# Performance work log

Hardware: AMD Instinct MI355X
Metric: run time of the kernel (lower is better)

Reference implementation:

```python
import jax, jax.numpy as jnp
import numpy as np

HEADS = 8
HEAD_DIM = 64
EPS = 1e-5


def setup_inputs() -> dict:
    key = jax.random.key(0)
    k1, k2, k3 = jax.random.split(key, 3)
    dim, hidden = 512, HEADS * HEAD_DIM
    x = jax.random.normal(k1, (8, dim, 64, 64), dtype=jnp.float32)
    w_qkv = jax.random.normal(k2, (hidden * 3, dim), dtype=jnp.float32) * (dim ** -0.5)
    w_out = jax.random.normal(k3, (dim, hidden), dtype=jnp.float32) * (hidden ** -0.5)
    b_out = jnp.zeros((dim,), dtype=jnp.float32)
    g = jnp.ones((dim,), dtype=jnp.float32)
    return {"x": x, "w_qkv": w_qkv, "w_out": w_out, "b_out": b_out, "g": g}


def reference(x, w_qkv, w_out, b_out, g):
    b, c, h, w = x.shape
    n = h * w
    scale = HEAD_DIM ** -0.5
    xf = x.reshape(b, c, n)  # 1x1 conv == channel matmul
    qkv = jnp.einsum('oc,bcn->bon', w_qkv, xf)
    q, k, v = jnp.split(qkv, 3, axis=1)
    def to_heads(t):
        return t.reshape(b, HEADS, HEAD_DIM, n)
    q, k, v = to_heads(q), to_heads(k), to_heads(v)
    q = jax.nn.softmax(q, axis=-2) * scale   # softmax over head_dim
    k = jax.nn.softmax(k, axis=-1)           # softmax over tokens
    v = v / n
    # context: (B,H,d,d) = k (B,H,d,N) @ v^T (B,H,N,e)
    context = jnp.einsum('bhdn,bhen->bhde', k, v)
    # out: context^T (e,d) @ q (d,N) -> (B,H,e,N)
    out = jnp.einsum('bhde,bhdn->bhen', context, q)
    out = out.reshape(b, HEADS * HEAD_DIM, n)
    y = jnp.einsum('co,bon->bcn', w_out, out) + b_out[None, :, None]
    # channel LayerNorm (mean/var over dim=1, biased var, scale g only)
    mean = jnp.mean(y, axis=1, keepdims=True)
    var = jnp.var(y, axis=1, keepdims=True)
    y = (y - mean) * jax.lax.rsqrt(var + EPS) * g[None, :, None]
    return y.reshape(b, c, h, w)
```

## Files before the change

### kernel.cpp

```cpp
#include <hip/hip_runtime.h>
#include <math.h>

#define BB 8
#define NN 4096
#define CD 512
#define HH 8
#define DD 64
#define OC3 1536
#define NSPLIT 16

typedef _Float16 f16;
typedef _Float16 half8 __attribute__((ext_vector_type(8)));
typedef _Float16 half4v __attribute__((ext_vector_type(4)));
typedef float f32x4 __attribute__((ext_vector_type(4)));

__device__ __forceinline__ void gload_lds16(const void* g, void* l) {
    __builtin_amdgcn_global_load_lds(
        (const __attribute__((address_space(1))) unsigned int*)g,
        (__attribute__((address_space(3))) unsigned int*)l, 16, 0, 0);
}

__global__ __launch_bounds__(256) void split_w_kernel(
    const float* __restrict__ w, f16* __restrict__ wh, f16* __restrict__ wl)
{
    int idx = blockIdx.x * 256 + threadIdx.x;
    float4 v = ((const float4*)w)[idx];
    float a[4] = {v.x, v.y, v.z, v.w};
    half4v h, l;
    #pragma unroll
    for (int i = 0; i < 4; ++i) {
        float s = a[i] * 64.f;
        f16 hh = (f16)s;
        h[i] = hh;
        l[i] = (f16)(s - (float)hh);
    }
    *(half4v*)(&wh[(long)idx * 4]) = h;
    *(half4v*)(&wl[(long)idx * 4]) = l;
}

__global__ __launch_bounds__(256) void split_x_kernel(
    const float* __restrict__ x, f16* __restrict__ xth, f16* __restrict__ xtl)
{
    __shared__ float tile[64][65];
    int b = blockIdx.z;
    int n0 = blockIdx.x * 64, c0 = blockIdx.y * 64;
    const float* xb = x + ((long)b * CD + c0) * NN + n0;
    int t = threadIdx.x;
    int tr = t >> 6, tc = t & 63;
    #pragma unroll
    for (int i = 0; i < 16; ++i)
        tile[tr + i * 4][tc] = xb[(long)(tr + i * 4) * NN + tc];
    __syncthreads();

    int nl = t >> 3, ck = (t & 7) * 8;
    long obase = ((long)b * NN + n0) * CD + c0;
    #pragma unroll
    for (int p = 0; p < 2; ++p) {
        int n = nl + p * 32;
        half8 h, l;
        #pragma unroll
        for (int j = 0; j < 8; ++j) {
            float s = tile[ck + j][n] * 16.f;
            f16 hv = (f16)s;
            h[j] = hv;
            l[j] = (f16)(s - (float)hv);
        }
        *(half8*)(&xth[obase + (long)n * CD + ck]) = h;
        *(half8*)(&xtl[obase + (long)n * CD + ck]) = l;
    }
}

#define STAGE(Lb, k0s)  do {                                                   \
    long kb_ = (long)(k0s) * 2;                                                \
    _Pragma("unroll")                                                          \
    for (int c_ = 0; c_ < 2; ++c_) {                                           \
        long rowoff_ = (long)(rb0 + c_ * 16) * 1024;                           \
        long ldsoff_ = (long)(rb0 + c_ * 16) * 64;                             \
        gload_lds16(gA_h + rowoff_ + kb_ + g_lane, (Lb) + 0 * 8192 + ldsoff_); \
        gload_lds16(gA_l + rowoff_ + kb_ + g_lane, (Lb) + 1 * 8192 + ldsoff_); \
        gload_lds16(gB_h + rowoff_ + kb_ + g_lane, (Lb) + 2 * 8192 + ldsoff_); \
        gload_lds16(gB_l + rowoff_ + kb_ + g_lane, (Lb) + 3 * 8192 + ldsoff_); \
    } } while (0)

__global__ __launch_bounds__(256) void mfma_gemm_kernel(
    const f16* __restrict__ Ah, const f16* __restrict__ Al, long sA,
    const f16* __restrict__ Bh, const f16* __restrict__ Bl, long sB,
    float* __restrict__ Cp, long sC, int ldC,
    const float* __restrict__ bias, const float* __restrict__ inv_sc,
    float base_sc, int fuseqv)
{
    __shared__ f16 lds[2][4][128 * 32];
    int bz = blockIdx.z;
    int n0 = blockIdx.x * 128, m0 = blockIdx.y * 128;
    int t = threadIdx.x;
    int lane = t & 63, wid = t >> 6;
    int wy = wid >> 1, wx = wid & 1;

    int cl = (lane & 3) ^ ((lane >> 3) & 3);
    long g_lane = (long)(lane >> 2) * 1024 + (long)cl * 16;

    const char* gA_h = (const char*)(Ah + bz * sA) + (long)m0 * 1024;
    const char* gA_l = (const char*)(Al + bz * sA) + (long)m0 * 1024;
    const char* gB_h = (const char*)(Bh + bz * sB) + (long)n0 * 1024;
    const char* gB_l = (const char*)(Bl + bz * sB) + (long)n0 * 1024;

    char* L0 = (char*)&lds[0][0][0];
    int rb0 = wid * 32;

    int cp = (lane >> 4) ^ (((lane & 15) >> 1) & 3);
    long offA = (long)(wy * 64 + (lane & 15)) * 64 + (long)cp * 16;
    long offB = (long)(wx * 64 + (lane & 15)) * 64 + (long)cp * 16;

    f32x4 acc[4][4];
    #pragma unroll
    for (int i = 0; i < 4; ++i)
        #pragma unroll
        for (int j = 0; j < 4; ++j)
            acc[i][j] = (f32x4){0.f, 0.f, 0.f, 0.f};

    STAGE(L0, 0);
    asm volatile("s_waitcnt vmcnt(0)" ::: "memory");
    __syncthreads();

    for (int s = 0; s < 16; ++s) {
        char* Lc = L0 + ((s & 1) << 15);
        if (s < 15) {
            char* Ln = L0 + (((s + 1) & 1) << 15);
            STAGE(Ln, (s + 1) * 32);
        }

        half8 ah[4], al[4], bh[4], bl[4];
        #pragma unroll
        for (int i = 0; i < 4; ++i) {
            ah[i] = *(const half8*)(Lc + 0 * 8192 + offA + i * 1024);
            al[i] = *(const half8*)(Lc + 1 * 8192 + offA + i * 1024);
            bh[i] = *(const half8*)(Lc + 2 * 8192 + offB + i * 1024);
            bl[i] = *(const half8*)(Lc + 3 * 8192 + offB + i * 1024);
        }
        #pragma unroll
        for (int i = 0; i < 4; ++i)
            #pragma unroll
            for (int j = 0; j < 4; ++j) {
                acc[i][j] = __builtin_amdgcn_mfma_f32_16x16x32_f16(ah[i], bh[j], acc[i][j], 0, 0, 0);
                acc[i][j] = __builtin_amdgcn_mfma_f32_16x16x32_f16(ah[i], bl[j], acc[i][j], 0, 0, 0);
                acc[i][j] = __builtin_amdgcn_mfma_f32_16x16x32_f16(al[i], bh[j], acc[i][j], 0, 0, 0);
            }

        asm volatile("s_waitcnt vmcnt(0)" ::: "memory");
        __syncthreads();
    }

    int colb = n0 + wx * 64 + (lane & 15);
    int rowb = m0 + wy * 64 + ((lane >> 4) << 2);

    if (fuseqv && m0 < 512) {
        int h = (m0 >> 6) + wy;
        f16* qh_b = (f16*)(Cp + (long)bz * sC);
        f16* ql_b = qh_b + (long)CD * NN;
        #pragma unroll
        for (int i = 0; i < 4; ++i)
            #pragma unroll
            for (int j = 0; j < 4; ++j)
                #pragma unroll
                for (int r = 0; r < 4; ++r)
                    acc[i][j][r] *= base_sc;
        #pragma unroll
        for (int j = 0; j < 4; ++j) {
            float mx = -INFINITY;
            #pragma unroll
            for (int i = 0; i < 4; ++i)
                #pragma unroll
                for (int r = 0; r < 4; ++r)
                    mx = fmaxf(mx, acc[i][j][r]);
            mx = fmaxf(mx, __shfl_xor(mx, 16));
            mx = fmaxf(mx, __shfl_xor(mx, 32));
            float sum = 0.f;
            #pragma unroll
            for (int i = 0; i < 4; ++i)
                #pragma unroll
                for (int r = 0; r < 4; ++r) {
                    float e = expf(acc[i][j][r] - mx);
                    acc[i][j][r] = e;
                    sum += e;
                }
            sum += __shfl_xor(sum, 16);
            sum += __shfl_xor(sum, 32);
            float rj = 32.f / sum;
            long nj = colb + j * 16;
            long off = nj * CD + h * 64 + ((lane >> 4) << 2);
            #pragma unroll
            for (int i = 0; i < 4; ++i) {
                half4v hh, ll;
                #pragma unroll
                for (int r = 0; r < 4; ++r) {
                    float v = acc[i][j][r] * rj;
                    f16 hv = (f16)v;
                    hh[r] = hv;
                    ll[r] = (f16)(v - (float)hv);
                }
                *(half4v*)(qh_b + off + i * 16) = hh;
                *(half4v*)(ql_b + off + i * 16) = ll;
            }
        }
        return;
    }

    if (fuseqv && m0 >= 1024) {
        f16* vhp = (f16*)(Cp + (long)bz * sC + 2L * CD * NN);
        f16* vlp = vhp + (long)CD * NN;
        float vsc = base_sc * 16.f;
        #pragma unroll
        for (int i = 0; i < 4; ++i)
            #pragma unroll
            for (int j = 0; j < 4; ++j)
                #pragma unroll
                for (int r = 0; r < 4; ++r) {
                    long row = rowb + i * 16 + r - 1024;
                    float val = acc[i][j][r] * vsc;
                    f16 hv = (f16)val;
                    vhp[row * NN + colb + j * 16] = hv;
                    vlp[row * NN + colb + j * 16] = (f16)(val - (float)hv);
                }
        return;
    }

    float* outp = Cp + bz * sC;
    float mult = base_sc * (inv_sc ? inv_sc[bz] : 1.f);
    #pragma unroll
    for (int i = 0; i < 4; ++i)
        #pragma unroll
        for (int j = 0; j < 4; ++j)
            #pragma unroll
            for (int r = 0; r < 4; ++r) {
                int row = rowb + i * 16 + r;
                float bb = bias ? bias[row] : 0.f;
                outp[(long)row * ldC + colb + j * 16] = acc[i][j][r] * mult + bb;
            }
}

__global__ __launch_bounds__(256) void softmax_k_kernel(
    const float* __restrict__ qkv, f16* __restrict__ ksp)
{
    int row = blockIdx.x;
    int b = row >> 9;
    int hd = row & (CD - 1);
    const float* base = qkv + ((long)b * OC3 + CD + hd) * NN;
    f16* khb = ksp + (long)b * 2 * CD * NN + (long)hd * NN;
    f16* klb = khb + (long)CD * NN;
    int t = threadIdx.x;

    float v[16];
    #pragma unroll
    for (int i = 0; i < 16; ++i) v[i] = base[t + i * 256];

    __shared__ float red[256];
    float mx = -INFINITY;
    #pragma unroll
    for (int i = 0; i < 16; ++i) mx = fmaxf(mx, v[i]);
    red[t] = mx; __syncthreads();
    for (int off = 128; off > 0; off >>= 1) {
        if (t < off) red[t] = fmaxf(red[t], red[t + off]);
        __syncthreads();
    }
    mx = red[0]; __syncthreads();

    float s = 0.f;
    #pragma unroll
    for (int i = 0; i < 16; ++i) {
        v[i] = expf(v[i] - mx);
        s += v[i];
    }
    red[t] = s; __syncthreads();
    for (int off = 128; off > 0; off >>= 1) {
        if (t < off) red[t] += red[t + off];
        __syncthreads();
    }
    float inv = 4096.f / red[0];

    #pragma unroll
    for (int i = 0; i < 16; ++i) {
        float val = v[i] * inv;
        f16 hv = (f16)val;
        khb[t + i * 256] = hv;
        klb[t + i * 256] = (f16)(val - (float)hv);
    }
}

__global__ __launch_bounds__(256) void ctx_mfma_kernel(
    const f16* __restrict__ ksp, const float* __restrict__ qkv,
    float* __restrict__ ctxp)
{
    __shared__ f16 lds[4][64 * 32];
    int sp = blockIdx.x;
    int bh = blockIdx.y;
    int b = bh >> 3, h = bh & 7;
    int t = threadIdx.x, lane = t & 63, w = t >> 6;

    const char* khg = (const char*)(ksp + (long)b * 2 * CD * NN) + (long)h * 64 * (NN * 2);
    const char* klg = khg + (long)CD * NN * 2;
    const char* vhg = (const char*)(qkv + ((long)b * OC3 + 2L * CD) * NN) + (long)h * 64 * (NN * 2);
    const char* vlg = vhg + (long)CD * NN * 2;
    const char* gw = (w == 0) ? khg : (w == 1) ? klg : (w == 2) ? vhg : vlg;

    int cl = (lane & 3) ^ ((lane >> 3) & 3);
    char* larr = (char*)&lds[0][0] + w * 4096;
    char* L = (char*)&lds[0][0];
    int cp16 = ((lane >> 4) ^ (((lane & 15) >> 1) & 3)) * 16;
    int lr = lane & 15;

    f32x4 acc[4];
    #pragma unroll
    for (int i = 0; i < 4; ++i) acc[i] = (f32x4){0.f, 0.f, 0.f, 0.f};

    for (int ks = 0; ks < 8; ++ks) {
        long kbyte = ((long)sp * 256 + ks * 32) * 2;
        #pragma unroll
        for (int c = 0; c < 4; ++c)
            gload_lds16(gw + (long)(c * 16 + (lane >> 2)) * (NN * 2) + kbyte + (long)cl * 16,
                        larr + c * 1024 + lane * 16);
        asm volatile("s_waitcnt vmcnt(0)" ::: "memory");
        __syncthreads();

        half8 ah[4], al[4], bhf, blf;
        #pragma unroll
        for (int i = 0; i < 4; ++i) {
            ah[i] = *(const half8*)(L + 0 * 4096 + (i * 16 + lr) * 64 + cp16);
            al[i] = *(const half8*)(L + 1 * 4096 + (i * 16 + lr) * 64 + cp16);
        }
        bhf = *(const half8*)(L + 2 * 4096 + (w * 16 + lr) * 64 + cp16);
        blf = *(const half8*)(L + 3 * 4096 + (w * 16 + lr) * 64 + cp16);
        #pragma unroll
        for (int i = 0; i < 4; ++i) {
            acc[i] = __builtin_amdgcn_mfma_f32_16x16x32_f16(ah[i], bhf, acc[i], 0, 0, 0);
            acc[i] = __builtin_amdgcn_mfma_f32_16x16x32_f16(ah[i], blf, acc[i], 0, 0, 0);
            acc[i] = __builtin_amdgcn_mfma_f32_16x16x32_f16(al[i], bhf, acc[i], 0, 0, 0);
        }
        __syncthreads();
    }

    float* op = ctxp + ((long)bh * NSPLIT + sp) * 4096;
    #pragma unroll
    for (int i = 0; i < 4; ++i)
        #pragma unroll
        for (int r = 0; r < 4; ++r)
            op[(i * 16 + (lane >> 4) * 4 + r) * 64 + w * 16 + lr] = acc[i][r];
}

__global__ __launch_bounds__(256) void context_reduce_kernel(
    const float* __restrict__ ctxp, float* __restrict__ ctx)
{
    int idx = blockIdx.x * 256 + threadIdx.x;
    int bh = idx >> 12;
    int de = idx & 4095;
    double s = 0.0;
    #pragma unroll
    for (int sp = 0; sp < NSPLIT; ++sp)
        s += (double)ctxp[((long)bh * NSPLIT + sp) * 4096 + de];
    ctx[idx] = (float)(s * (1.0 / 268435456.0));
}

__global__ __launch_bounds__(256) void fold_wout_kernel(
    const float* __restrict__ w_out, const float* __restrict__ ctx,
    float* __restrict__ Mf)
{
    __shared__ float cl[64][65];
    int ct = blockIdx.x;
    int bh = blockIdx.y;
    int b = bh >> 3, h = bh & 7;
    int t = threadIdx.x;
    const float* cp = ctx + (long)bh * 4096;
    #pragma unroll
    for (int i = 0; i < 16; ++i) {
        int o = t + i * 256;
        cl[o >> 6][o & 63] = cp[o];
    }
    __syncthreads();

    int d = t & 63, tc = t >> 6;
    #pragma unroll 4
    for (int ci = 0; ci < 32; ++ci) {
        int c = ct * 128 + tc * 32 + ci;
        const float* wr = w_out + (long)c * CD + h * DD;
        float s = 0.f;
        #pragma unroll
        for (int e = 0; e < 64; ++e) s += wr[e] * cl[d][e];
        Mf[((long)b * CD + c) * CD + h * DD + d] = s;
    }
}

__global__ __launch_bounds__(256) void max_m_part_kernel(
    const float* __restrict__ Mf, float* __restrict__ part)
{
    int blk = blockIdx.x;
    int b = blk >> 5, sub = blk & 31;
    const float4* p = (const float4*)(Mf + (long)b * CD * CD) + (long)sub * 2048;
    float mx = 0.f;
    for (int i = threadIdx.x; i < 2048; i += 256) {
        float4 v = p[i];
        mx = fmaxf(mx, fmaxf(fmaxf(fabsf(v.x), fabsf(v.y)),
                             fmaxf(fabsf(v.z), fabsf(v.w))));
    }
    __shared__ float red[256];
    red[threadIdx.x] = mx; __syncthreads();
    for (int off = 128; off > 0; off >>= 1) {
        if (threadIdx.x < off) red[threadIdx.x] = fmaxf(red[threadIdx.x], red[threadIdx.x + off]);
        __syncthreads();
    }
    if (threadIdx.x == 0) part[blk] = red[0];
}

__global__ __launch_bounds__(64) void max_m_final_kernel(
    const float* __restrict__ part, float* __restrict__ scl)
{
    int b = threadIdx.x;
    if (b < 8) {
        float m = 0.f;
        #pragma unroll
        for (int i = 0; i < 32; ++i) m = fmaxf(m, part[b * 32 + i]);
        int e = (m > 1e-30f) ? ilogbf(m) : 0;
        scl[b] = ldexpf(1.f, 10 - e);
        scl[8 + b] = ldexpf(1.f, e - 10);
    }
}

__global__ __launch_bounds__(256) void split_m_kernel(
    const float* __restrict__ Mf, const float* __restrict__ scl,
    f16* __restrict__ mh, f16* __restrict__ ml)
{
    int idx = blockIdx.x * 256 + threadIdx.x;
    float s = scl[idx >> 16];
    float4 v = ((const float4*)Mf)[idx];
    float a[4] = {v.x, v.y, v.z, v.w};
    half4v h, l;
    #pragma unroll
    for (int i = 0; i < 4; ++i) {
        float tval = a[i] * s;
        f16 hv = (f16)tval;
        h[i] = hv;
        l[i] = (f16)(tval - (float)hv);
    }
    *(half4v*)(&mh[(long)idx * 4]) = h;
    *(half4v*)(&ml[(long)idx * 4]) = l;
}

__global__ __launch_bounds__(256) void layernorm_kernel(
    const float* __restrict__ qkv, const float* __restrict__ g,
    float* __restrict__ out)
{
    int t = threadIdx.x;
    int tn = t & 31, cy = t >> 5;
    long col = (long)blockIdx.x * 32 + tn;
    int n = (int)(col & (NN - 1));
    int b = (int)(col >> 12);
    const float* base = qkv + (long)b * OC3 * NN + (long)CD * NN + n;

    float v[64];
    double s = 0.0, ss = 0.0;
    #pragma unroll
    for (int i = 0; i < 64; ++i) {
        v[i] = base[(long)(cy * 64 + i) * NN];
        s += (double)v[i];
        ss += (double)v[i] * (double)v[i];
    }

    __shared__ double rs[8][32], rss[8][32];
    rs[cy][tn] = s; rss[cy][tn] = ss;
    __syncthreads();
    __shared__ float mb[32], ib[32];
    if (cy == 0) {
        double S = 0.0, SS = 0.0;
        #pragma unroll
        for (int j = 0; j < 8; ++j) { S += rs[j][tn]; SS += rss[j][tn]; }
        double mean = S * (1.0 / CD);
        double var = SS * (1.0 / CD) - mean * mean;
        mb[tn] = (float)mean;
        ib[tn] = (float)(1.0 / sqrt(var + 1e-5));
    }
    __syncthreads();
    float m = mb[tn], iv = ib[tn];

    float* oc = out + (long)b * CD * NN + n;
    #pragma unroll
    for (int i = 0; i < 64; ++i)
        oc[(long)(cy * 64 + i) * NN] = (v[i] - m) * iv * g[cy * 64 + i];
}

extern "C" void kernel_launch(void* const* d_in, const int* in_sizes, int n_in,
                              void* d_out, int out_size, void* d_ws, size_t ws_size,
                              hipStream_t stream)
{
    const float* x     = (const float*)d_in[0];
    const float* w_qkv = (const float*)d_in[1];
    const float* w_out = (const float*)d_in[2];
    const float* b_out = (const float*)d_in[3];
    const float* g     = (const float*)d_in[4];
    float* out = (float*)d_out;

    float* ws   = (float*)d_ws;
    float* qkv  = ws;
    float* ctxp = qkv + (long)BB * OC3 * NN;
    float* ctx  = ctxp + (long)BB * HH * NSPLIT * DD * DD;
    f16*   mh   = (f16*)(ctx + (long)BB * HH * DD * DD);
    f16*   ml   = mh + (long)BB * CD * CD;
    f16*   wh   = (f16*)(ml + (long)BB * CD * CD);
    f16*   wl   = wh + (long)OC3 * CD;
    float* scl  = (float*)(wl + (long)OC3 * CD);
    float* part = scl + 16;
    float* Mf   = ctxp;

    f16* xth = (f16*)d_out;
    f16* xtl = xth + (long)BB * NN * CD;
    f16* ksp = (f16*)d_out;

    split_w_kernel<<<(OC3 * CD / 4) / 256, 256, 0, stream>>>(w_qkv, wh, wl);
    split_x_kernel<<<dim3(NN / 64, CD / 64, BB), 256, 0, stream>>>(x, xth, xtl);

    mfma_gemm_kernel<<<dim3(NN / 128, OC3 / 128, BB), 256, 0, stream>>>(
        wh, wl, 0L, xth, xtl, (long)NN * CD,
        qkv, (long)OC3 * NN, NN, nullptr, nullptr, 1.0f / 1024.0f, 1);

    softmax_k_kernel<<<BB * CD, 256, 0, stream>>>(qkv, ksp);

    ctx_mfma_kernel<<<dim3(NSPLIT, BB * HH), 256, 0, stream>>>(ksp, qkv, ctxp);
    context_reduce_kernel<<<(BB * HH * DD * DD) / 256, 256, 0, stream>>>(ctxp, ctx);

    fold_wout_kernel<<<dim3(4, BB * HH), 256, 0, stream>>>(w_out, ctx, Mf);
    max_m_part_kernel<<<256, 256, 0, stream>>>(Mf, part);
    max_m_final_kernel<<<1, 64, 0, stream>>>(part, scl);
    split_m_kernel<<<(BB * CD * CD / 4) / 256, 256, 0, stream>>>(Mf, scl, mh, ml);

    mfma_gemm_kernel<<<dim3(NN / 128, CD / 128, BB), 256, 0, stream>>>(
        mh, ml, (long)CD * CD,
        (const f16*)qkv, (const f16*)qkv + (long)CD * NN, (long)OC3 * NN * 2,
        qkv + (long)CD * NN, (long)OC3 * NN, NN, b_out, scl + 8, 1.0f / 256.0f,
        0);

    layernorm_kernel<<<(BB * NN) / 32, 256, 0, stream>>>(qkv, g, out);
}
```

Before: 415.2 us.

## Enlarge GEMM tiles to 256x256 with 512 threads and fuse context reduction into fold

The split-fp16 MFMA GEMM now uses 256x256 output tiles with 8 waves, each wave computing 128x64 and streaming B fragments per column, so each staged byte feeds more MFMAs. The q-softmax epilogue is adjusted to cover two heads per wave. The separate context reduction kernel is removed and folded into fold_wout, which now runs one block per batch-head and writes Mf into the output buffer. The larger tile uses 128KB of LDS and many more accumulator registers, and it launches far fewer blocks (e.g. 16x2x8 for the output GEMM), which risks low occupancy. The fold kernel also has less parallelism.

```diff
diff --git a/kernel.cpp b/kernel.cpp
--- a/kernel.cpp
+++ b/kernel.cpp
@@ -70,31 +70,34 @@
     }
 }
 
+#define AR  16384
+#define BUF 65536
+
 #define STAGE(Lb, k0s)  do {                                                   \
     long kb_ = (long)(k0s) * 2;                                                \
     _Pragma("unroll")                                                          \
     for (int c_ = 0; c_ < 2; ++c_) {                                           \
         long rowoff_ = (long)(rb0 + c_ * 16) * 1024;                           \
         long ldsoff_ = (long)(rb0 + c_ * 16) * 64;                             \
-        gload_lds16(gA_h + rowoff_ + kb_ + g_lane, (Lb) + 0 * 8192 + ldsoff_); \
-        gload_lds16(gA_l + rowoff_ + kb_ + g_lane, (Lb) + 1 * 8192 + ldsoff_); \
-        gload_lds16(gB_h + rowoff_ + kb_ + g_lane, (Lb) + 2 * 8192 + ldsoff_); \
-        gload_lds16(gB_l + rowoff_ + kb_ + g_lane, (Lb) + 3 * 8192 + ldsoff_); \
+        gload_lds16(gA_h + rowoff_ + kb_ + g_lane, (Lb) + 0 * AR + ldsoff_);   \
+        gload_lds16(gA_l + rowoff_ + kb_ + g_lane, (Lb) + 1 * AR + ldsoff_);   \
+        gload_lds16(gB_h + rowoff_ + kb_ + g_lane, (Lb) + 2 * AR + ldsoff_);   \
+        gload_lds16(gB_l + rowoff_ + kb_ + g_lane, (Lb) + 3 * AR + ldsoff_);   \
     } } while (0)
 
-__global__ __launch_bounds__(256) void mfma_gemm_kernel(
+__global__ __launch_bounds__(512, 2) void mfma_gemm_kernel(
     const f16* __restrict__ Ah, const f16* __restrict__ Al, long sA,
     const f16* __restrict__ Bh, const f16* __restrict__ Bl, long sB,
     float* __restrict__ Cp, long sC, int ldC,
     const float* __restrict__ bias, const float* __restrict__ inv_sc,
     float base_sc, int fuseqv)
 {
-    __shared__ f16 lds[2][4][128 * 32];
+    __shared__ f16 lds[2][4][256 * 32];
     int bz = blockIdx.z;
-    int n0 = blockIdx.x * 128, m0 = blockIdx.y * 128;
+    int n0 = blockIdx.x * 256, m0 = blockIdx.y * 256;
     int t = threadIdx.x;
     int lane = t & 63, wid = t >> 6;
-    int wy = wid >> 1, wx = wid & 1;
+    int wy = wid >> 2, wx = wid & 3;
 
     int cl = (lane & 3) ^ ((lane >> 3) & 3);
     long g_lane = (long)(lane >> 2) * 1024 + (long)cl * 16;
@@ -108,12 +111,12 @@
     int rb0 = wid * 32;
 
     int cp = (lane >> 4) ^ (((lane & 15) >> 1) & 3);
-    long offA = (long)(wy * 64 + (lane & 15)) * 64 + (long)cp * 16;
+    long offA = (long)(wy * 128 + (lane & 15)) * 64 + (long)cp * 16;
     long offB = (long)(wx * 64 + (lane & 15)) * 64 + (long)cp * 16;
 
-    f32x4 acc[4][4];
-    #pragma unroll
-    for (int i = 0; i < 4; ++i)
+    f32x4 acc[8][4];
+    #pragma unroll
+    for (int i = 0; i < 8; ++i)
         #pragma unroll
         for (int j = 0; j < 4; ++j)
             acc[i][j] = (f32x4){0.f, 0.f, 0.f, 0.f};
@@ -123,42 +126,43 @@
     __syncthreads();
 
     for (int s = 0; s < 16; ++s) {
-        char* Lc = L0 + ((s & 1) << 15);
+        char* Lc = L0 + ((s & 1) ? BUF : 0);
         if (s < 15) {
-            char* Ln = L0 + (((s + 1) & 1) << 15);
+            char* Ln = L0 + (((s + 1) & 1) ? BUF : 0);
             STAGE(Ln, (s + 1) * 32);
         }
 
-        half8 ah[4], al[4], bh[4], bl[4];
-        #pragma unroll
-        for (int i = 0; i < 4; ++i) {
-            ah[i] = *(const half8*)(Lc + 0 * 8192 + offA + i * 1024);
-            al[i] = *(const half8*)(Lc + 1 * 8192 + offA + i * 1024);
-            bh[i] = *(const half8*)(Lc + 2 * 8192 + offB + i * 1024);
-            bl[i] = *(const half8*)(Lc + 3 * 8192 + offB + i * 1024);
-        }
-        #pragma unroll
-        for (int i = 0; i < 4; ++i)
+        half8 ah[8], al[8];
+        #pragma unroll
+        for (int i = 0; i < 8; ++i) {
+            ah[i] = *(const half8*)(Lc + 0 * AR + offA + i * 1024);
+            al[i] = *(const half8*)(Lc + 1 * AR + offA + i * 1024);
+        }
+        #pragma unroll
+        for (int j = 0; j < 4; ++j) {
+            half8 bh = *(const half8*)(Lc + 2 * AR + offB + j * 1024);
+            half8 bl = *(const half8*)(Lc + 3 * AR + offB + j * 1024);
             #pragma unroll
-            for (int j = 0; j < 4; ++j) {
-                acc[i][j] = __builtin_amdgcn_mfma_f32_16x16x32_f16(ah[i], bh[j], acc[i][j], 0, 0, 0);
-                acc[i][j] = __builtin_amdgcn_mfma_f32_16x16x32_f16(ah[i], bl[j], acc[i][j], 0, 0, 0);
-                acc[i][j] = __builtin_amdgcn_mfma_f32_16x16x32_f16(al[i], bh[j], acc[i][j], 0, 0, 0);
+            for (int i = 0; i < 8; ++i) {
+                acc[i][j] = __builtin_amdgcn_mfma_f32_16x16x32_f16(ah[i], bh, acc[i][j], 0, 0, 0);
+                acc[i][j] = __builtin_amdgcn_mfma_f32_16x16x32_f16(ah[i], bl, acc[i][j], 0, 0, 0);
+                acc[i][j] = __builtin_amdgcn_mfma_f32_16x16x32_f16(al[i], bh, acc[i][j], 0, 0, 0);
             }
+        }
 
         asm volatile("s_waitcnt vmcnt(0)" ::: "memory");
         __syncthreads();
     }
 
     int colb = n0 + wx * 64 + (lane & 15);
-    int rowb = m0 + wy * 64 + ((lane >> 4) << 2);
+    int rowb = m0 + wy * 128 + ((lane >> 4) << 2);
 
     if (fuseqv && m0 < 512) {
-        int h = (m0 >> 6) + wy;
+        int h0 = (m0 >> 6) + wy * 2;
         f16* qh_b = (f16*)(Cp + (long)bz * sC);
         f16* ql_b = qh_b + (long)CD * NN;
         #pragma unroll
-        for (int i = 0; i < 4; ++i)
+        for (int i = 0; i < 8; ++i)
             #pragma unroll
             for (int j = 0; j < 4; ++j)
                 #pragma unroll
@@ -166,40 +170,43 @@
                     acc[i][j][r] *= base_sc;
         #pragma unroll
         for (int j = 0; j < 4; ++j) {
-            float mx = -INFINITY;
+            long nj = colb + j * 16;
             #pragma unroll
-            for (int i = 0; i < 4; ++i)
+            for (int g = 0; g < 2; ++g) {
+                float mx = -INFINITY;
                 #pragma unroll
-                for (int r = 0; r < 4; ++r)
-                    mx = fmaxf(mx, acc[i][j][r]);
-            mx = fmaxf(mx, __shfl_xor(mx, 16));
-            mx = fmaxf(mx, __shfl_xor(mx, 32));
-            float sum = 0.f;
-            #pragma unroll
-            for (int i = 0; i < 4; ++i)
+                for (int di = 0; di < 4; ++di)
+                    #pragma unroll
+                    for (int r = 0; r < 4; ++r)
+                        mx = fmaxf(mx, acc[g * 4 + di][j][r]);
+                mx = fmaxf(mx, __shfl_xor(mx, 16));
+                mx = fmaxf(mx, __shfl_xor(mx, 32));
+                float sum = 0.f;
                 #pragma unroll
-                for (int r = 0; r < 4; ++r) {
-                    float e = expf(acc[i][j][r] - mx);
-                    acc[i][j][r] = e;
-                    sum += e;
+                for (int di = 0; di < 4; ++di)
+                    #pragma unroll
+                    for (int r = 0; r < 4; ++r) {
+                        float e = expf(acc[g * 4 + di][j][r] - mx);
+                        acc[g * 4 + di][j][r] = e;
+                        sum += e;
+                    }
+                sum += __shfl_xor(sum, 16);
+                sum += __shfl_xor(sum, 32);
+                float rj = 32.f / sum;
+                long off = nj * CD + (h0 + g) * 64 + ((lane >> 4) << 2);
+                #pragma unroll
+                for (int di = 0; di < 4; ++di) {
+                    half4v hh, ll;
+                    #pragma unroll
+                    for (int r = 0; r < 4; ++r) {
+                        float v = acc[g * 4 + di][j][r] * rj;
+                        f16 hv = (f16)v;
+                        hh[r] = hv;
+                        ll[r] = (f16)(v - (float)hv);
+                    }
+                    *(half4v*)(qh_b + off + di * 16) = hh;
+                    *(half4v*)(ql_b + off + di * 16) = ll;
                 }
-            sum += __shfl_xor(sum, 16);
-            sum += __shfl_xor(sum, 32);
-            float rj = 32.f / sum;
-            long nj = colb + j * 16;
-            long off = nj * CD + h * 64 + ((lane >> 4) << 2);
-            #pragma unroll
-            for (int i = 0; i < 4; ++i) {
-                half4v hh, ll;
-                #pragma unroll
-                for (int r = 0; r < 4; ++r) {
-                    float v = acc[i][j][r] * rj;
-                    f16 hv = (f16)v;
-                    hh[r] = hv;
-                    ll[r] = (f16)(v - (float)hv);
-                }
-                *(half4v*)(qh_b + off + i * 16) = hh;
-                *(half4v*)(ql_b + off + i * 16) = ll;
             }
         }
         return;
@@ -210,7 +217,7 @@
         f16* vlp = vhp + (long)CD * NN;
         float vsc = base_sc * 16.f;
         #pragma unroll
-        for (int i = 0; i < 4; ++i)
+        for (int i = 0; i < 8; ++i)
             #pragma unroll
             for (int j = 0; j < 4; ++j)
                 #pragma unroll
@@ -227,7 +234,7 @@
     float* outp = Cp + bz * sC;
     float mult = base_sc * (inv_sc ? inv_sc[bz] : 1.f);
     #pragma unroll
-    for (int i = 0; i < 4; ++i)
+    for (int i = 0; i < 8; ++i)
         #pragma unroll
         for (int j = 0; j < 4; ++j)
             #pragma unroll
@@ -346,40 +353,29 @@
             op[(i * 16 + (lane >> 4) * 4 + r) * 64 + w * 16 + lr] = acc[i][r];
 }
 
-__global__ __launch_bounds__(256) void context_reduce_kernel(
-    const float* __restrict__ ctxp, float* __restrict__ ctx)
-{
-    int idx = blockIdx.x * 256 + threadIdx.x;
-    int bh = idx >> 12;
-    int de = idx & 4095;
-    double s = 0.0;
-    #pragma unroll
-    for (int sp = 0; sp < NSPLIT; ++sp)
-        s += (double)ctxp[((long)bh * NSPLIT + sp) * 4096 + de];
-    ctx[idx] = (float)(s * (1.0 / 268435456.0));
-}
-
 __global__ __launch_bounds__(256) void fold_wout_kernel(
-    const float* __restrict__ w_out, const float* __restrict__ ctx,
+    const float* __restrict__ w_out, const float* __restrict__ ctxp,
     float* __restrict__ Mf)
 {
     __shared__ float cl[64][65];
-    int ct = blockIdx.x;
-    int bh = blockIdx.y;
+    int bh = blockIdx.x;
     int b = bh >> 3, h = bh & 7;
     int t = threadIdx.x;
-    const float* cp = ctx + (long)bh * 4096;
+    const float* cp = ctxp + (long)bh * NSPLIT * 4096;
     #pragma unroll
     for (int i = 0; i < 16; ++i) {
-        int o = t + i * 256;
-        cl[o >> 6][o & 63] = cp[o];
+        int de = t + i * 256;
+        double s = 0.0;
+        #pragma unroll
+        for (int sp = 0; sp < NSPLIT; ++sp)
+            s += (double)cp[(long)sp * 4096 + de];
+        cl[de >> 6][de & 63] = (float)(s * (1.0 / 268435456.0));
     }
     __syncthreads();
 
     int d = t & 63, tc = t >> 6;
-    #pragma unroll 4
-    for (int ci = 0; ci < 32; ++ci) {
-        int c = ct * 128 + tc * 32 + ci;
+    for (int ci = 0; ci < 128; ++ci) {
+        int c = tc * 128 + ci;
         const float* wr = w_out + (long)c * CD + h * DD;
         float s = 0.f;
         #pragma unroll
@@ -499,37 +495,35 @@
     float* ws   = (float*)d_ws;
     float* qkv  = ws;
     float* ctxp = qkv + (long)BB * OC3 * NN;
-    float* ctx  = ctxp + (long)BB * HH * NSPLIT * DD * DD;
-    f16*   mh   = (f16*)(ctx + (long)BB * HH * DD * DD);
+    f16*   mh   = (f16*)(ctxp + (long)BB * HH * NSPLIT * DD * DD);
     f16*   ml   = mh + (long)BB * CD * CD;
     f16*   wh   = (f16*)(ml + (long)BB * CD * CD);
     f16*   wl   = wh + (long)OC3 * CD;
     float* scl  = (float*)(wl + (long)OC3 * CD);
     float* part = scl + 16;
-    float* Mf   = ctxp;
 
     f16* xth = (f16*)d_out;
     f16* xtl = xth + (long)BB * NN * CD;
     f16* ksp = (f16*)d_out;
+    float* Mf = (float*)d_out;
 
     split_w_kernel<<<(OC3 * CD / 4) / 256, 256, 0, stream>>>(w_qkv, wh, wl);
     split_x_kernel<<<dim3(NN / 64, CD / 64, BB), 256, 0, stream>>>(x, xth, xtl);
 
-    mfma_gemm_kernel<<<dim3(NN / 128, OC3 / 128, BB), 256, 0, stream>>>(
+    mfma_gemm_kernel<<<dim3(NN / 256, OC3 / 256, BB), 512, 0, stream>>>(
         wh, wl, 0L, xth, xtl, (long)NN * CD,
         qkv, (long)OC3 * NN, NN, nullptr, nullptr, 1.0f / 1024.0f, 1);
 
     softmax_k_kernel<<<BB * CD, 256, 0, stream>>>(qkv, ksp);
 
     ctx_mfma_kernel<<<dim3(NSPLIT, BB * HH), 256, 0, stream>>>(ksp, qkv, ctxp);
-    context_reduce_kernel<<<(BB * HH * DD * DD) / 256, 256, 0, stream>>>(ctxp, ctx);
-
-    fold_wout_kernel<<<dim3(4, BB * HH), 256, 0, stream>>>(w_out, ctx, Mf);
+
+    fold_wout_kernel<<<BB * HH, 256, 0, stream>>>(w_out, ctxp, Mf);
     max_m_part_kernel<<<256, 256, 0, stream>>>(Mf, part);
     max_m_final_kernel<<<1, 64, 0, stream>>>(part, scl);
     split_m_kernel<<<(BB * CD * CD / 4) / 256, 256, 0, stream>>>(Mf, scl, mh, ml);
 
-    mfma_gemm_kernel<<<dim3(NN / 128, CD / 128, BB), 256, 0, stream>>>(
+    mfma_gemm_kernel<<<dim3(NN / 256, CD / 256, BB), 512, 0, stream>>>(
         mh, ml, (long)CD * CD,
         (const f16*)qkv, (const f16*)qkv + (long)CD * NN, (long)OC3 * NN * 2,
         qkv + (long)CD * NN, (long)OC3 * NN, NN, b_out, scl + 8, 1.0f / 256.0f,
```

New measurement: 423.4 us. No clear change (+2.0%).
